# Performance work log

Measured on AMD Instinct MI355X. Metric: run time of the kernel, lower is better.

Reference implementation:

```python
import jax, jax.numpy as jnp
import numpy as np

BS, N_GENES, N_FEAT = 4, 15135, 64
HIDDEN, NUM_LAYERS = 128, 2
HIDDEN_FC, N_CMT, N_CLASSES = 256, 1000, 10
N_EDGES = 100000


def _linear_params(k, din, dout):
    # torch.nn.Linear default init: U(-1/sqrt(din), 1/sqrt(din))
    s = 1.0 / np.sqrt(din)
    kw, kb = jax.random.split(k)
    W = jax.random.uniform(kw, (din, dout), jnp.float32, -s, s)
    b = jax.random.uniform(kb, (dout,), jnp.float32, -s, s)
    return W, b


def setup_inputs() -> dict:
    key = jax.random.key(0)
    ks = jax.random.split(key, 9)
    W1, b1 = _linear_params(ks[0], N_FEAT, HIDDEN)
    W2, b2 = _linear_params(ks[1], HIDDEN, HIDDEN)
    Wfc, bfc = _linear_params(ks[2], NUM_LAYERS * HIDDEN, 1)
    Wl1, bl1 = _linear_params(ks[3], N_CMT, HIDDEN_FC)
    Wl2, bl2 = _linear_params(ks[4], HIDDEN_FC, N_CLASSES)
    x = jax.random.normal(ks[5], (BS, N_GENES, N_FEAT), jnp.float32)
    row = jax.random.randint(ks[6], (N_EDGES,), 0, N_GENES)
    col = jax.random.randint(ks[7], (N_EDGES,), 0, N_CMT)
    batch = jnp.zeros((BS,), jnp.int32)  # accepted but unused by forward
    return dict(x=x, batch=batch, row=row, col=col,
                W1=W1, b1=b1, W2=W2, b2=b2, Wfc=Wfc, bfc=bfc,
                Wl1=Wl1, bl1=bl1, Wl2=Wl2, bl2=bl2)


def reference(x, batch, row, col, W1, b1, W2, b2, Wfc, bfc, Wl1, bl1, Wl2, bl2):
    bs, n = x.shape[0], x.shape[1]
    # MLP stack (mode='cat', no batchnorm)
    h1 = jax.nn.relu(jnp.einsum('bnf,fh->bnh', x, W1) + b1)   # [bs, n, H]
    h2 = jax.nn.relu(jnp.einsum('bnh,hk->bnk', h1, W2) + b2)  # [bs, n, H]
    # torch.stack(xs, -1).view(bs, n, -1): layers interleaved per hidden unit
    feat = jnp.stack([h1, h2], axis=-1).reshape(bs, n, -1)    # [bs, n, 2H]
    # pathway pooling: gather nodes by row, segment-mean into n_cmt groups
    g = jnp.transpose(feat, (1, 0, 2))[row]                   # [E, bs, 2H]
    seg_sum = jax.ops.segment_sum(g, col, num_segments=N_CMT)          # [n_cmt, bs, 2H]
    cnt = jax.ops.segment_sum(jnp.ones_like(col, feat.dtype), col,
                              num_segments=N_CMT)                      # [n_cmt]
    seg_mean = seg_sum / jnp.maximum(cnt, 1.0)[:, None, None]          # empty segs -> 0
    pooled = jnp.transpose(seg_mean, (1, 0, 2)).reshape(-1, feat.shape[-1])  # [bs*n_cmt, 2H]
    scores = (pooled @ Wfc + bfc).reshape(-1, N_CMT)          # [bs, n_cmt]
    # head (eval mode: dropout is identity)
    h = jax.nn.relu(scores @ Wl1 + bl1)                       # [bs, hidden_fc]
    logits = h @ Wl2 + bl2                                    # [bs, n_classes]
    return jax.nn.log_softmax(logits, axis=-1)
```

## Files before the change

kernel.cpp:

```cpp
#include <hip/hip_runtime.h>
#include <hip/hip_bf16.h>

#define BSZ   4
#define NG    15135
#define MROWS (BSZ*NG)
#define NF    64
#define H     128
#define NCMT  1000
#define NEDGE 100000
#define HFC   256
#define NCLS  10
#define NB    64
#define PSTR  5120
#define CCH   25

typedef __attribute__((ext_vector_type(8))) short  bfrag;
typedef __attribute__((ext_vector_type(4))) float  f32x4;

__device__ __forceinline__ unsigned int pkbf(float a, float b) {
    union { __hip_bfloat162 h2; unsigned int u; } c;
    c.h2 = __float22bfloat162_rn(make_float2(a, b));
    return c.u;
}

__global__ __launch_bounds__(256) void kP(const float* __restrict__ W1,
                                          const float* __restrict__ W2,
                                          const float* __restrict__ bl1,
                                          unsigned int* __restrict__ wfrag_u32,
                                          float* __restrict__ hacc) {
    const int q = blockIdx.x * 256 + threadIdx.x;
    if (q < BSZ * HFC) hacc[q] = bl1[q & (HFC - 1)];

    const int e = 2 * q;
    float f0, f1;
    if (e < 8192) {
        const int kk = e & 7, l = (e >> 3) & 63, ct = e >> 9;
        const int t = ct & 1, ci = ct >> 1;
        const int k = t * 32 + (l >> 4) * 8 + kk;
        const int i = ci * 16 + (l & 15);
        f0 = W1[k * H + i];
        f1 = W1[(k + 1) * H + i];
    } else {
        const int e2 = e - 8192;
        const int kk = e2 & 7, l = (e2 >> 3) & 63, ct = e2 >> 9;
        const int t = ct & 3, ci = ct >> 2;
        const int k = t * 32 + (l >> 4) * 8 + kk;
        const int i = ci * 16 + (l & 15);
        f0 = W2[k * H + i];
        f1 = W2[(k + 1) * H + i];
    }
    wfrag_u32[q] = pkbf(f0, f1);
}

__global__ __launch_bounds__(256, 2) void k1_fdot(const float* __restrict__ x,
                                                  const unsigned int* __restrict__ wfrag_g,
                                                  const float* __restrict__ b1,
                                                  const float* __restrict__ b2,
                                                  const float* __restrict__ Wfc,
                                                  float* __restrict__ fdot4) {
    __shared__ unsigned int   wfrag[12288];
    __shared__ unsigned short h1s[4][16][136];

    const int tid  = threadIdx.x;
    const int lane = tid & 63, wid = tid >> 6;
    const int sub  = lane & 15, grp = lane >> 4;
    const int r  = blockIdx.x * 64 + wid * 16 + sub;
    const int rc = r < MROWS ? r : MROWS - 1;

    float4 xr[4];
    #pragma unroll
    for (int t = 0; t < 2; ++t) {
        xr[2 * t]     = *(const float4*)&x[(size_t)rc * NF + t * 32 + grp * 8];
        xr[2 * t + 1] = *(const float4*)&x[(size_t)rc * NF + t * 32 + grp * 8 + 4];
    }

    {
        const uint4* src = (const uint4*)wfrag_g;
        uint4* dst = (uint4*)wfrag;
        #pragma unroll
        for (int i = 0; i < 12; ++i) dst[i * 256 + tid] = src[i * 256 + tid];
    }
    __syncthreads();

    bfrag bx[2];
    #pragma unroll
    for (int t = 0; t < 2; ++t) {
        union { bfrag v; unsigned int u[4]; } pk;
        const float4 a = xr[2 * t], b = xr[2 * t + 1];
        pk.u[0] = pkbf(a.x, a.y); pk.u[1] = pkbf(a.z, a.w);
        pk.u[2] = pkbf(b.x, b.y); pk.u[3] = pkbf(b.z, b.w);
        bx[t] = pk.v;
    }

    const bfrag* w1f = (const bfrag*)wfrag;
    const bfrag* w2f = (const bfrag*)(wfrag + 4096);
    float fp = 0.f;

    #pragma unroll
    for (int ci = 0; ci < 8; ++ci) {
        f32x4 c1 = {0.f, 0.f, 0.f, 0.f};
        c1 = __builtin_amdgcn_mfma_f32_16x16x32_bf16(w1f[(ci * 2 + 0) * 64 + lane], bx[0], c1, 0, 0, 0);
        c1 = __builtin_amdgcn_mfma_f32_16x16x32_bf16(w1f[(ci * 2 + 1) * 64 + lane], bx[1], c1, 0, 0, 0);
        const int c0 = ci * 16 + grp * 4;
        const float4 b1v = *(const float4*)&b1[c0];
        const float4 wfa = *(const float4*)&Wfc[2 * c0];
        const float4 wfb = *(const float4*)&Wfc[2 * c0 + 4];
        const float h0 = fmaxf(c1[0] + b1v.x, 0.f);
        const float h1 = fmaxf(c1[1] + b1v.y, 0.f);
        const float h2 = fmaxf(c1[2] + b1v.z, 0.f);
        const float h3 = fmaxf(c1[3] + b1v.w, 0.f);
        fp = fmaf(h0, wfa.x, fp); fp = fmaf(h1, wfa.z, fp);
        fp = fmaf(h2, wfb.x, fp); fp = fmaf(h3, wfb.z, fp);
        *(uint2*)&h1s[wid][sub][c0] = make_uint2(pkbf(h0, h1), pkbf(h2, h3));
    }

    bfrag bh[4];
    #pragma unroll
    for (int t = 0; t < 4; ++t)
        bh[t] = *(const bfrag*)&h1s[wid][sub][t * 32 + grp * 8];

    #pragma unroll
    for (int ci = 0; ci < 8; ++ci) {
        f32x4 c2 = {0.f, 0.f, 0.f, 0.f};
        #pragma unroll
        for (int t = 0; t < 4; ++t)
            c2 = __builtin_amdgcn_mfma_f32_16x16x32_bf16(w2f[(ci * 4 + t) * 64 + lane], bh[t], c2, 0, 0, 0);
        const int c0 = ci * 16 + grp * 4;
        const float4 b2v = *(const float4*)&b2[c0];
        const float4 wfa = *(const float4*)&Wfc[2 * c0];
        const float4 wfb = *(const float4*)&Wfc[2 * c0 + 4];
        fp = fmaf(fmaxf(c2[0] + b2v.x, 0.f), wfa.y, fp);
        fp = fmaf(fmaxf(c2[1] + b2v.y, 0.f), wfa.w, fp);
        fp = fmaf(fmaxf(c2[2] + b2v.z, 0.f), wfb.y, fp);
        fp = fmaf(fmaxf(c2[3] + b2v.w, 0.f), wfb.w, fp);
    }

    fp += __shfl_xor(fp, 16);
    fp += __shfl_xor(fp, 32);
    if (grp == 0 && r < MROWS) {
        const int b = r / NG, g = r - b * NG;
        fdot4[g * 4 + b] = fp;
    }
}

__global__ __launch_bounds__(512) void k2_scatter(const int* __restrict__ row,
                                                  const int* __restrict__ col,
                                                  const float* __restrict__ fdot4,
                                                  float* __restrict__ partial) {
    __shared__ float lacc[4 * NCMT];
    __shared__ int   lcnt[NCMT];
    const int tid = threadIdx.x;
    #pragma unroll
    for (int i = tid; i < 4 * NCMT; i += 512) lacc[i] = 0.f;
    #pragma unroll
    for (int i = tid; i < NCMT; i += 512) lcnt[i] = 0;
    __syncthreads();

    for (int e = blockIdx.x * 512 + tid; e < NEDGE; e += NB * 512) {
        const int r = row[e];
        const int c = col[e];
        const float4 f = *(const float4*)&fdot4[r * 4];
        unsafeAtomicAdd(&lacc[c],            f.x);
        unsafeAtomicAdd(&lacc[NCMT + c],     f.y);
        unsafeAtomicAdd(&lacc[2 * NCMT + c], f.z);
        unsafeAtomicAdd(&lacc[3 * NCMT + c], f.w);
        atomicAdd(&lcnt[c], 1);
    }
    __syncthreads();

    float* dst = partial + (size_t)blockIdx.x * PSTR;
    #pragma unroll
    for (int i = tid; i < 4 * NCMT; i += 512) dst[i] = lacc[i];
    #pragma unroll
    for (int i = tid; i < NCMT; i += 512) dst[4 * NCMT + i] = (float)lcnt[i];
}

__global__ __launch_bounds__(256) void k3a_head1(const float* __restrict__ partial,
                                                 const float* __restrict__ bfc,
                                                 const float* __restrict__ Wl1,
                                                 float* __restrict__ hacc) {
    __shared__ float tmp[5][CCH];
    __shared__ float sc[BSZ][CCH];
    const int c0 = blockIdx.x * CCH;
    const int t = threadIdx.x;

    if (t < 5 * CCH) {
        const int v = t / CCH, cc = t % CCH;
        float s = 0.f;
        #pragma unroll 8
        for (int blk = 0; blk < NB; ++blk)
            s += partial[(size_t)blk * PSTR + v * NCMT + c0 + cc];
        tmp[v][cc] = s;
    }
    __syncthreads();
    if (t < BSZ * CCH) {
        const int b = t / CCH, cc = t % CCH;
        sc[b][cc] = tmp[b][cc] / fmaxf(tmp[4][cc], 1.f) + bfc[0];
    }
    __syncthreads();

    float p0 = 0.f, p1 = 0.f, p2 = 0.f, p3 = 0.f;
    #pragma unroll
    for (int cc = 0; cc < CCH; ++cc) {
        const float wv = Wl1[(size_t)(c0 + cc) * HFC + t];
        p0 = fmaf(sc[0][cc], wv, p0);
        p1 = fmaf(sc[1][cc], wv, p1);
        p2 = fmaf(sc[2][cc], wv, p2);
        p3 = fmaf(sc[3][cc], wv, p3);
    }
    unsafeAtomicAdd(&hacc[0 * HFC + t], p0);
    unsafeAtomicAdd(&hacc[1 * HFC + t], p1);
    unsafeAtomicAdd(&hacc[2 * HFC + t], p2);
    unsafeAtomicAdd(&hacc[3 * HFC + t], p3);
}

__global__ __launch_bounds__(64) void k3b_head2(const float* __restrict__ hacc,
                                                const float* __restrict__ Wl2,
                                                const float* __restrict__ bl2,
                                                float* __restrict__ out) {
    __shared__ float lg[BSZ][NCLS];
    const int t = threadIdx.x;
    if (t < BSZ * NCLS) {
        const int b = t / NCLS, k = t % NCLS;
        float a = bl2[k];
        for (int j = 0; j < HFC; ++j)
            a = fmaf(fmaxf(hacc[b * HFC + j], 0.f), Wl2[j * NCLS + k], a);
        lg[b][k] = a;
    }
    __syncthreads();
    if (t < BSZ * NCLS) {
        const int b = t / NCLS, k = t % NCLS;
        float m = lg[b][0];
        #pragma unroll
        for (int k2 = 1; k2 < NCLS; ++k2) m = fmaxf(m, lg[b][k2]);
        float s = 0.f;
        #pragma unroll
        for (int k2 = 0; k2 < NCLS; ++k2) s += expf(lg[b][k2] - m);
        out[b * NCLS + k] = lg[b][k] - m - logf(s);
    }
}

extern "C" void kernel_launch(void* const* d_in, const int* in_sizes, int n_in,
                              void* d_out, int out_size, void* d_ws, size_t ws_size,
                              hipStream_t stream) {
    const float* x   = (const float*)d_in[0];
    const int*   row = (const int*)d_in[2];
    const int*   col = (const int*)d_in[3];
    const float* W1  = (const float*)d_in[4];
    const float* b1  = (const float*)d_in[5];
    const float* W2  = (const float*)d_in[6];
    const float* b2  = (const float*)d_in[7];
    const float* Wfc = (const float*)d_in[8];
    const float* bfc = (const float*)d_in[9];
    const float* Wl1 = (const float*)d_in[10];
    const float* bl1 = (const float*)d_in[11];
    const float* Wl2 = (const float*)d_in[12];
    const float* bl2 = (const float*)d_in[13];

    float* ws      = (float*)d_ws;
    float* fdot4   = ws;
    float* partial = ws + 60544;
    float* hacc    = ws + 388224;
    unsigned int* wfrag = (unsigned int*)(ws + 389248);

    kP<<<48, 256, 0, stream>>>(W1, W2, bl1, wfrag, hacc);
    k1_fdot<<<(MROWS + 63) / 64, 256, 0, stream>>>(x, wfrag, b1, b2, Wfc, fdot4);
    k2_scatter<<<NB, 512, 0, stream>>>(row, col, fdot4, partial);
    k3a_head1<<<NCMT / CCH, 256, 0, stream>>>(partial, bfc, Wl1, hacc);
    k3b_head2<<<1, 64, 0, stream>>>(hacc, Wl2, bl2, (float*)d_out);
}
```

Measured before the change: 45.47 us.

## Fuse weight packing into MLP kernel and replace head atomics with partial buffers

New measurement: 65.94 us. 45.0% more time.

```diff
diff --git a/kernel.cpp b/kernel.cpp
--- a/kernel.cpp
+++ b/kernel.cpp
@@ -10,9 +10,10 @@
 #define NEDGE 100000
 #define HFC   256
 #define NCLS  10
-#define NB    64
+#define NB    32
 #define PSTR  5120
 #define CCH   25
+#define NHP   40
 
 typedef __attribute__((ext_vector_type(8))) short  bfrag;
 typedef __attribute__((ext_vector_type(4))) float  f32x4;
@@ -23,37 +24,9 @@
     return c.u;
 }
 
-__global__ __launch_bounds__(256) void kP(const float* __restrict__ W1,
-                                          const float* __restrict__ W2,
-                                          const float* __restrict__ bl1,
-                                          unsigned int* __restrict__ wfrag_u32,
-                                          float* __restrict__ hacc) {
-    const int q = blockIdx.x * 256 + threadIdx.x;
-    if (q < BSZ * HFC) hacc[q] = bl1[q & (HFC - 1)];
-
-    const int e = 2 * q;
-    float f0, f1;
-    if (e < 8192) {
-        const int kk = e & 7, l = (e >> 3) & 63, ct = e >> 9;
-        const int t = ct & 1, ci = ct >> 1;
-        const int k = t * 32 + (l >> 4) * 8 + kk;
-        const int i = ci * 16 + (l & 15);
-        f0 = W1[k * H + i];
-        f1 = W1[(k + 1) * H + i];
-    } else {
-        const int e2 = e - 8192;
-        const int kk = e2 & 7, l = (e2 >> 3) & 63, ct = e2 >> 9;
-        const int t = ct & 3, ci = ct >> 2;
-        const int k = t * 32 + (l >> 4) * 8 + kk;
-        const int i = ci * 16 + (l & 15);
-        f0 = W2[k * H + i];
-        f1 = W2[(k + 1) * H + i];
-    }
-    wfrag_u32[q] = pkbf(f0, f1);
-}
-
 __global__ __launch_bounds__(256, 2) void k1_fdot(const float* __restrict__ x,
-                                                  const unsigned int* __restrict__ wfrag_g,
+                                                  const float* __restrict__ W1,
+                                                  const float* __restrict__ W2,
                                                   const float* __restrict__ b1,
                                                   const float* __restrict__ b2,
                                                   const float* __restrict__ Wfc,
@@ -74,11 +47,28 @@
         xr[2 * t + 1] = *(const float4*)&x[(size_t)rc * NF + t * 32 + grp * 8 + 4];
     }
 
-    {
-        const uint4* src = (const uint4*)wfrag_g;
-        uint4* dst = (uint4*)wfrag;
-        #pragma unroll
-        for (int i = 0; i < 12; ++i) dst[i * 256 + tid] = src[i * 256 + tid];
+    #pragma unroll
+    for (int i = 0; i < 48; ++i) {
+        const int q = i * 256 + tid;
+        const int e = 2 * q;
+        float f0, f1;
+        if (i < 16) {
+            const int kk = e & 7, l = (e >> 3) & 63, ct = e >> 9;
+            const int t = ct & 1, ci = ct >> 1;
+            const int k = t * 32 + (l >> 4) * 8 + kk;
+            const int ii = ci * 16 + (l & 15);
+            f0 = W1[k * H + ii];
+            f1 = W1[(k + 1) * H + ii];
+        } else {
+            const int e2 = e - 8192;
+            const int kk = e2 & 7, l = (e2 >> 3) & 63, ct = e2 >> 9;
+            const int t = ct & 3, ci = ct >> 2;
+            const int k = t * 32 + (l >> 4) * 8 + kk;
+            const int ii = ci * 16 + (l & 15);
+            f0 = W2[k * H + ii];
+            f1 = W2[(k + 1) * H + ii];
+        }
+        wfrag[q] = pkbf(f0, f1);
     }
     __syncthreads();
 
@@ -143,20 +133,19 @@
     }
 }
 
-__global__ __launch_bounds__(512) void k2_scatter(const int* __restrict__ row,
-                                                  const int* __restrict__ col,
-                                                  const float* __restrict__ fdot4,
-                                                  float* __restrict__ partial) {
+__global__ __launch_bounds__(1024) void k2_scatter(const int* __restrict__ row,
+                                                   const int* __restrict__ col,
+                                                   const float* __restrict__ fdot4,
+                                                   float* __restrict__ partial) {
     __shared__ float lacc[4 * NCMT];
     __shared__ int   lcnt[NCMT];
     const int tid = threadIdx.x;
     #pragma unroll
-    for (int i = tid; i < 4 * NCMT; i += 512) lacc[i] = 0.f;
-    #pragma unroll
-    for (int i = tid; i < NCMT; i += 512) lcnt[i] = 0;
-    __syncthreads();
-
-    for (int e = blockIdx.x * 512 + tid; e < NEDGE; e += NB * 512) {
+    for (int i = tid; i < 4 * NCMT; i += 1024) lacc[i] = 0.f;
+    if (tid < NCMT) lcnt[tid] = 0;
+    __syncthreads();
+
+    for (int e = blockIdx.x * 1024 + tid; e < NEDGE; e += NB * 1024) {
         const int r = row[e];
         const int c = col[e];
         const float4 f = *(const float4*)&fdot4[r * 4];
@@ -170,15 +159,14 @@
 
     float* dst = partial + (size_t)blockIdx.x * PSTR;
     #pragma unroll
-    for (int i = tid; i < 4 * NCMT; i += 512) dst[i] = lacc[i];
-    #pragma unroll
-    for (int i = tid; i < NCMT; i += 512) dst[4 * NCMT + i] = (float)lcnt[i];
+    for (int i = tid; i < 4 * NCMT; i += 1024) dst[i] = lacc[i];
+    if (tid < NCMT) dst[4 * NCMT + tid] = (float)lcnt[tid];
 }
 
 __global__ __launch_bounds__(256) void k3a_head1(const float* __restrict__ partial,
                                                  const float* __restrict__ bfc,
                                                  const float* __restrict__ Wl1,
-                                                 float* __restrict__ hacc) {
+                                                 float* __restrict__ hp) {
     __shared__ float tmp[5][CCH];
     __shared__ float sc[BSZ][CCH];
     const int c0 = blockIdx.x * CCH;
@@ -208,23 +196,38 @@
         p2 = fmaf(sc[2][cc], wv, p2);
         p3 = fmaf(sc[3][cc], wv, p3);
     }
-    unsafeAtomicAdd(&hacc[0 * HFC + t], p0);
-    unsafeAtomicAdd(&hacc[1 * HFC + t], p1);
-    unsafeAtomicAdd(&hacc[2 * HFC + t], p2);
-    unsafeAtomicAdd(&hacc[3 * HFC + t], p3);
-}
-
-__global__ __launch_bounds__(64) void k3b_head2(const float* __restrict__ hacc,
-                                                const float* __restrict__ Wl2,
-                                                const float* __restrict__ bl2,
-                                                float* __restrict__ out) {
+    float* dst = hp + (size_t)blockIdx.x * (BSZ * HFC);
+    dst[0 * HFC + t] = p0;
+    dst[1 * HFC + t] = p1;
+    dst[2 * HFC + t] = p2;
+    dst[3 * HFC + t] = p3;
+}
+
+__global__ __launch_bounds__(256) void k3b_head2(const float* __restrict__ hp,
+                                                 const float* __restrict__ bl1,
+                                                 const float* __restrict__ Wl2,
+                                                 const float* __restrict__ bl2,
+                                                 float* __restrict__ out) {
+    __shared__ float hrelu[BSZ][HFC];
     __shared__ float lg[BSZ][NCLS];
     const int t = threadIdx.x;
+
+    #pragma unroll
+    for (int q = 0; q < BSZ; ++q) {
+        float s = 0.f;
+        #pragma unroll 8
+        for (int blk = 0; blk < NHP; ++blk)
+            s += hp[(size_t)blk * (BSZ * HFC) + q * HFC + t];
+        hrelu[q][t] = fmaxf(s + bl1[t], 0.f);
+    }
+    __syncthreads();
+
     if (t < BSZ * NCLS) {
         const int b = t / NCLS, k = t % NCLS;
         float a = bl2[k];
+        #pragma unroll 4
         for (int j = 0; j < HFC; ++j)
-            a = fmaf(fmaxf(hacc[b * HFC + j], 0.f), Wl2[j * NCLS + k], a);
+            a = fmaf(hrelu[b][j], Wl2[j * NCLS + k], a);
         lg[b][k] = a;
     }
     __syncthreads();
@@ -260,12 +263,10 @@
     float* ws      = (float*)d_ws;
     float* fdot4   = ws;
     float* partial = ws + 60544;
-    float* hacc    = ws + 388224;
-    unsigned int* wfrag = (unsigned int*)(ws + 389248);
-
-    kP<<<48, 256, 0, stream>>>(W1, W2, bl1, wfrag, hacc);
-    k1_fdot<<<(MROWS + 63) / 64, 256, 0, stream>>>(x, wfrag, b1, b2, Wfc, fdot4);
-    k2_scatter<<<NB, 512, 0, stream>>>(row, col, fdot4, partial);
-    k3a_head1<<<NCMT / CCH, 256, 0, stream>>>(partial, bfc, Wl1, hacc);
-    k3b_head2<<<1, 64, 0, stream>>>(hacc, Wl2, bl2, (float*)d_out);
-}
+    float* hp      = ws + 224384;
+
+    k1_fdot<<<(MROWS + 63) / 64, 256, 0, stream>>>(x, W1, W2, b1, b2, Wfc, fdot4);
+    k2_scatter<<<NB, 1024, 0, stream>>>(row, col, fdot4, partial);
+    k3a_head1<<<NCMT / CCH, 256, 0, stream>>>(partial, bfc, Wl1, hp);
+    k3b_head2<<<1, 256, 0, stream>>>(hp, bl1, Wl2, bl2, (float*)d_out);
+}
```

## Fuse head kernels via last-block counter and reduce scatter partials with atomics

Applied to the files above, without the earlier changes.

Result: slower. 58.37 us (+28.4%).

```diff
diff --git a/kernel.cpp b/kernel.cpp
--- a/kernel.cpp
+++ b/kernel.cpp
@@ -10,9 +10,9 @@
 #define NEDGE 100000
 #define HFC   256
 #define NCLS  10
-#define NB    64
-#define PSTR  5120
+#define NB    40
 #define CCH   25
+#define NCH   40
 
 typedef __attribute__((ext_vector_type(8))) short  bfrag;
 typedef __attribute__((ext_vector_type(4))) float  f32x4;
@@ -25,11 +25,14 @@
 
 __global__ __launch_bounds__(256) void kP(const float* __restrict__ W1,
                                           const float* __restrict__ W2,
-                                          const float* __restrict__ bl1,
                                           unsigned int* __restrict__ wfrag_u32,
-                                          float* __restrict__ hacc) {
+                                          float* __restrict__ acc,
+                                          int* __restrict__ cnt,
+                                          int* __restrict__ ctr) {
     const int q = blockIdx.x * 256 + threadIdx.x;
-    if (q < BSZ * HFC) hacc[q] = bl1[q & (HFC - 1)];
+    if (q < BSZ * NCMT) acc[q] = 0.f;
+    if (q < NCMT)       cnt[q] = 0;
+    if (q == 0)         ctr[0] = 0;
 
     const int e = 2 * q;
     float f0, f1;
@@ -146,13 +149,13 @@
 __global__ __launch_bounds__(512) void k2_scatter(const int* __restrict__ row,
                                                   const int* __restrict__ col,
                                                   const float* __restrict__ fdot4,
-                                                  float* __restrict__ partial) {
+                                                  float* __restrict__ acc,
+                                                  int* __restrict__ cnt) {
     __shared__ float lacc[4 * NCMT];
     __shared__ int   lcnt[NCMT];
     const int tid = threadIdx.x;
     #pragma unroll
     for (int i = tid; i < 4 * NCMT; i += 512) lacc[i] = 0.f;
-    #pragma unroll
     for (int i = tid; i < NCMT; i += 512) lcnt[i] = 0;
     __syncthreads();
 
@@ -168,34 +171,32 @@
     }
     __syncthreads();
 
-    float* dst = partial + (size_t)blockIdx.x * PSTR;
-    #pragma unroll
-    for (int i = tid; i < 4 * NCMT; i += 512) dst[i] = lacc[i];
-    #pragma unroll
-    for (int i = tid; i < NCMT; i += 512) dst[4 * NCMT + i] = (float)lcnt[i];
-}
-
-__global__ __launch_bounds__(256) void k3a_head1(const float* __restrict__ partial,
+    #pragma unroll
+    for (int i = tid; i < 4 * NCMT; i += 512)
+        unsafeAtomicAdd(&acc[i], lacc[i]);
+    for (int i = tid; i < NCMT; i += 512)
+        atomicAdd(&cnt[i], lcnt[i]);
+}
+
+__global__ __launch_bounds__(256) void k3ab_head(const float* __restrict__ acc,
+                                                 const int* __restrict__ cnt,
                                                  const float* __restrict__ bfc,
                                                  const float* __restrict__ Wl1,
-                                                 float* __restrict__ hacc) {
-    __shared__ float tmp[5][CCH];
+                                                 const float* __restrict__ bl1,
+                                                 const float* __restrict__ Wl2,
+                                                 const float* __restrict__ bl2,
+                                                 float* __restrict__ hp,
+                                                 int* __restrict__ ctr,
+                                                 float* __restrict__ out) {
     __shared__ float sc[BSZ][CCH];
+    __shared__ int lastflag;
     const int c0 = blockIdx.x * CCH;
     const int t = threadIdx.x;
 
-    if (t < 5 * CCH) {
-        const int v = t / CCH, cc = t % CCH;
-        float s = 0.f;
-        #pragma unroll 8
-        for (int blk = 0; blk < NB; ++blk)
-            s += partial[(size_t)blk * PSTR + v * NCMT + c0 + cc];
-        tmp[v][cc] = s;
-    }
-    __syncthreads();
     if (t < BSZ * CCH) {
         const int b = t / CCH, cc = t % CCH;
-        sc[b][cc] = tmp[b][cc] / fmaxf(tmp[4][cc], 1.f) + bfc[0];
+        const int c = c0 + cc;
+        sc[b][cc] = acc[b * NCMT + c] / fmaxf((float)cnt[c], 1.f) + bfc[0];
     }
     __syncthreads();
 
@@ -208,23 +209,43 @@
         p2 = fmaf(sc[2][cc], wv, p2);
         p3 = fmaf(sc[3][cc], wv, p3);
     }
-    unsafeAtomicAdd(&hacc[0 * HFC + t], p0);
-    unsafeAtomicAdd(&hacc[1 * HFC + t], p1);
-    unsafeAtomicAdd(&hacc[2 * HFC + t], p2);
-    unsafeAtomicAdd(&hacc[3 * HFC + t], p3);
-}
-
-__global__ __launch_bounds__(64) void k3b_head2(const float* __restrict__ hacc,
-                                                const float* __restrict__ Wl2,
-                                                const float* __restrict__ bl2,
-                                                float* __restrict__ out) {
+    {
+        float* dst = hp + (size_t)blockIdx.x * (BSZ * HFC);
+        dst[0 * HFC + t] = p0;
+        dst[1 * HFC + t] = p1;
+        dst[2 * HFC + t] = p2;
+        dst[3 * HFC + t] = p3;
+    }
+
+    __threadfence();
+    __syncthreads();
+    if (t == 0) {
+        const int old = __hip_atomic_fetch_add(ctr, 1, __ATOMIC_ACQ_REL,
+                                               __HIP_MEMORY_SCOPE_AGENT);
+        lastflag = (old == NCH - 1);
+    }
+    __syncthreads();
+    if (!lastflag) return;
+    __threadfence();
+
+    __shared__ float hrelu[BSZ][HFC];
+    #pragma unroll
+    for (int q = 0; q < BSZ; ++q) {
+        float s = 0.f;
+        #pragma unroll 8
+        for (int blk = 0; blk < NCH; ++blk)
+            s += hp[(size_t)blk * (BSZ * HFC) + q * HFC + t];
+        hrelu[q][t] = fmaxf(s + bl1[t], 0.f);
+    }
+    __syncthreads();
+
     __shared__ float lg[BSZ][NCLS];
-    const int t = threadIdx.x;
     if (t < BSZ * NCLS) {
         const int b = t / NCLS, k = t % NCLS;
         float a = bl2[k];
+        #pragma unroll 4
         for (int j = 0; j < HFC; ++j)
-            a = fmaf(fmaxf(hacc[b * HFC + j], 0.f), Wl2[j * NCLS + k], a);
+            a = fmaf(hrelu[b][j], Wl2[j * NCLS + k], a);
         lg[b][k] = a;
     }
     __syncthreads();
@@ -257,15 +278,17 @@
     const float* Wl2 = (const float*)d_in[12];
     const float* bl2 = (const float*)d_in[13];
 
-    float* ws      = (float*)d_ws;
-    float* fdot4   = ws;
-    float* partial = ws + 60544;
-    float* hacc    = ws + 388224;
-    unsigned int* wfrag = (unsigned int*)(ws + 389248);
-
-    kP<<<48, 256, 0, stream>>>(W1, W2, bl1, wfrag, hacc);
+    float* ws    = (float*)d_ws;
+    float* fdot4 = ws;
+    float* acc   = ws + 60544;
+    int*   cnt   = (int*)(ws + 64544);
+    int*   ctr   = (int*)(ws + 65544);
+    float* hp    = ws + 65552;
+    unsigned int* wfrag = (unsigned int*)(ws + 106512);
+
+    kP<<<48, 256, 0, stream>>>(W1, W2, wfrag, acc, cnt, ctr);
     k1_fdot<<<(MROWS + 63) / 64, 256, 0, stream>>>(x, wfrag, b1, b2, Wfc, fdot4);
-    k2_scatter<<<NB, 512, 0, stream>>>(row, col, fdot4, partial);
-    k3a_head1<<<NCMT / CCH, 256, 0, stream>>>(partial, bfc, Wl1, hacc);
-    k3b_head2<<<1, 64, 0, stream>>>(hacc, Wl2, bl2, (float*)d_out);
-}
+    k2_scatter<<<NB, 512, 0, stream>>>(row, col, fdot4, acc, cnt);
+    k3ab_head<<<NCH, 256, 0, stream>>>(acc, cnt, bfc, Wl1, bl1, Wl2, bl2,
+                                       hp, ctr, (float*)d_out);
+}
```
